# Kernel optimization log

Hardware: AMD Instinct MI355X
Metric: run time of the kernel (lower is better)

The kernel has to match this reference:

```python
import jax, jax.numpy as jnp
import numpy as np

# Static config mirroring PyTorchConv1dAutograd(padding=0, index_back=500, out_size=None)
PADDING = 0
INDEX_BACK = 500


def next_power2(n):
    return 1 << (int(n) - 1).bit_length()


def setup_inputs() -> dict:
    key = jax.random.key(0)
    k1, k2, k3 = jax.random.split(key, 3)
    N, C, W = 32, 64, 4096
    F, WW = 128, 9
    x = jax.random.normal(k1, (N, C, W), dtype=jnp.float32)
    filt = jax.random.normal(k2, (F, C, WW), dtype=jnp.float32) * 0.1
    bias = jax.random.normal(k3, (F,), dtype=jnp.float32)
    return {"x": x, "filt": filt, "bias": bias}


def reference(x, filt, bias):
    N, C, W = x.shape
    F, _, WW = filt.shape
    p = PADDING
    out_W = W - WW + 1 + 2 * p
    WWW = max(out_W, WW)
    init_fft_size = next_power2(W + 2 * p + WWW - 1)

    # zero-pad input by `p` on the front; rfft pads the rest with zeros via n=
    if p > 0:
        x = jnp.pad(x, ((0, 0), (0, 0), (p, 0)))
    xfft = jnp.fft.rfft(x, n=init_fft_size, axis=-1)          # [N, C, half]
    yfft = jnp.fft.rfft(filt, n=init_fft_size, axis=-1)       # [F, C, half]

    half_fft_size = init_fft_size // 2 + 1
    half_compressed = half_fft_size - INDEX_BACK
    compress_fft_size = half_compressed * 2
    xfft = xfft[..., :half_compressed]
    yfft = yfft[..., :half_compressed]

    # cross-correlation in frequency domain: X * conj(Y), contract over channels
    spec = jnp.einsum('ncw,fcw->nfw', xfft, jnp.conj(yfft))   # [N, F, half_compressed]
    out = jnp.fft.irfft(spec, n=compress_fft_size, axis=-1)[..., :out_W]
    return out + bias[None, :, None]
```

## Files before the change

kernel.cpp:

```cpp
#include <hip/hip_runtime.h>
#include <hip/hip_bf16.h>

typedef unsigned short u16;
typedef unsigned int   u32;

using bf16x8 = __attribute__((ext_vector_type(8))) short;
using f32x4  = __attribute__((ext_vector_type(4))) float;

#define NB    32
#define CC    64
#define WW_   4096
#define FF    128
#define TAPS  9
#define KBINS 3597
#define N2    7194
#define OW    4088
#define SIG2  4096
#define JMAX  4104
#define KD    4160
#define XTROWS 4352
#define PBIG  58933248LL

__device__ __forceinline__ u16 f2bf(float f) {
    u32 u = __float_as_uint(f);
    return (u16)((u + 0x7FFFu + ((u >> 16) & 1u)) >> 16);
}
__device__ __forceinline__ float vsin(float x) {
    float r; asm("v_sin_f32 %0, %1" : "=v"(r) : "v"(x)); return r;
}

__device__ __forceinline__ void gload16(const void* g, void* l) {
    __builtin_amdgcn_global_load_lds(
        (const __attribute__((address_space(1))) void*)g,
        (__attribute__((address_space(3))) void*)l, 16, 0, 0);
}

__global__ __launch_bounds__(256) void cast_xt(const float* __restrict__ x,
                                               u16* __restrict__ XT) {
    __shared__ u16 tl[64][72];
    const int tid = threadIdx.x;
    const int it = blockIdx.x, n = blockIdx.y;
    const int i0 = it * 64;
    {
        int c = tid >> 2, io = (tid & 3) * 16;
        const float4* src = (const float4*)(x + ((size_t)n * CC + c) * WW_ +
                                            i0 + io);
#pragma unroll
        for (int q = 0; q < 4; q++) {
            float4 v = src[q];
            tl[c][io + q * 4 + 0] = f2bf(v.x);
            tl[c][io + q * 4 + 1] = f2bf(v.y);
            tl[c][io + q * 4 + 2] = f2bf(v.z);
            tl[c][io + q * 4 + 3] = f2bf(v.w);
        }
    }
    __syncthreads();
    {
        int l = tid >> 2;
        int R = i0 + l + 64;
        int key = R & 7;
        u16* dst = XT + ((size_t)n * XTROWS + R) * 64;
        int pb0 = (tid & 3) * 2;
#pragma unroll
        for (int pq = 0; pq < 2; pq++) {
            int pb = pb0 + pq;
            int ch0 = (pb ^ key) << 3;
            bf16x8 v;
#pragma unroll
            for (int ci = 0; ci < 8; ci++) v[ci] = (short)tl[ch0 + ci][l];
            *(bf16x8*)(dst + pb * 8) = v;
        }
    }
}

__global__ __launch_bounds__(256) void prep(const float* __restrict__ filt,
                                            u16* __restrict__ F2) {
    int idx = blockIdx.x * 256 + threadIdx.x;
    if (idx >= FF * 576) return;
    int f = idx / 576, wc = idx % 576;
    int w = wc >> 6, c = wc & 63;
    F2[idx] = f2bf(filt[((size_t)f * CC + c) * TAPS + w]);
}

__global__ __launch_bounds__(256) void gen_D(u16* __restrict__ D) {
    int t = blockIdx.x;
    u32* row = (u32*)(D + (size_t)t * KD);
    for (int p = threadIdx.x; p < KD / 2; p += 256) {
        u32 pack = 0;
#pragma unroll
        for (int e = 0; e < 2; e++) {
            int j = 2 * p + e;
            float d = 0.f;
            if (j < JMAX) {
                long long v = 8192LL * t - 7194LL * (long long)(j - 8);
                long long r = v % PBIG;
                if (r < 0) r += PBIG;
                if (r == 0) {
                    d = 7193.0f / 7194.0f;
                } else {
                    long long n64 = (7193LL * r) % (2LL * PBIG);
                    float num = vsin((float)n64 * (float)(0.5 / (double)PBIG));
                    long long rr = (r < PBIG - r) ? r : PBIG - r;
                    float den;
                    if (rr < (1LL << 18))
                        den = (float)rr *
                              (float)(3.14159265358979323846 / (double)PBIG);
                    else
                        den = vsin((float)r * (float)(0.5 / (double)PBIG));
                    d = num / (7194.0f * den);
                }
            }
            pack |= (u32)f2bf(d) << (16 * e);
        }
        row[p] = pack;
    }
}

#define STAGE_A9(T, BUF)                                                    \
    _Pragma("unroll")                                                       \
    for (int q = 0; q < 4; q++) {                                           \
        gload16(F2 + (size_t)(wid * 32 + q * 8 + (lane >> 3)) * 576 +       \
                    (T) * 64 + (((lane & 7) ^ (lane >> 3)) * 8),            \
                lac + (BUF)*16384 + (wid * 32 + q * 8) * 128);              \
    }

__global__ __launch_bounds__(256, 2) void conv9(const u16* __restrict__ XT,
                                                const u16* __restrict__ F2,
                                                u16* __restrict__ Z) {
    __shared__ u16 la[2 * 128 * 64];
    __shared__ u16 lx[96 * 64];
    const int tid = threadIdx.x;
    const int lane = tid & 63, wid = tid >> 6;
    const int jt = blockIdx.x, n = blockIdx.y;
    const int fr = lane & 15;
    const int hk = (lane >> 4) << 4;
    const int askew = (fr & 7) << 4;
    char* lac = (char*)la;
    char* lxc = (char*)lx;

    {
        const u16* src = XT + ((size_t)n * XTROWS + jt * 64 + 56) * 64;
#pragma unroll
        for (int q = 0; q < 3; q++) {
            int off = (wid * 3 + q) * 512;
            gload16(src + off + lane * 8, lxc + off * 2);
        }
    }
    STAGE_A9(0, 0)
    __syncthreads();

    f32x4 acc[2][4];
#pragma unroll
    for (int i = 0; i < 2; i++)
#pragma unroll
        for (int j = 0; j < 4; j++) acc[i][j] = (f32x4){0.f, 0.f, 0.f, 0.f};

    bf16x8 af[2][2], bfr[4][2];
    for (int t = 0; t < TAPS; ++t) {
        const int cur = t & 1, nxt = cur ^ 1;
#pragma unroll
        for (int m2 = 0; m2 < 2; m2++)
#pragma unroll
            for (int kk = 0; kk < 2; kk++) {
                int row_ = wid * 32 + m2 * 16 + fr;
                af[m2][kk] = *(const bf16x8*)(lac + cur * 16384 + row_ * 128 +
                                              ((kk * 64 + hk) ^ askew));
            }
#pragma unroll
        for (int n4 = 0; n4 < 4; n4++)
#pragma unroll
            for (int kk = 0; kk < 2; kk++) {
                int l_ = n4 * 16 + fr + t;
                bfr[n4][kk] = *(const bf16x8*)(lxc + l_ * 128 +
                                  ((kk * 64 + hk) ^ ((l_ & 7) << 4)));
            }
        if (t + 1 < TAPS) STAGE_A9(t + 1, nxt)
        __builtin_amdgcn_s_setprio(1);
#pragma unroll
        for (int kk = 0; kk < 2; kk++)
#pragma unroll
            for (int m2 = 0; m2 < 2; m2++)
#pragma unroll
                for (int n4 = 0; n4 < 4; n4++)
                    acc[m2][n4] = __builtin_amdgcn_mfma_f32_16x16x32_bf16(
                        af[m2][kk], bfr[n4][kk], acc[m2][n4], 0, 0, 0);
        __builtin_amdgcn_s_setprio(0);
        __syncthreads();
    }

#pragma unroll
    for (int m2 = 0; m2 < 2; m2++) {
#pragma unroll
        for (int n4 = 0; n4 < 4; n4++) {
            int colk = jt * 64 + n4 * 16 + fr;
            int f0 = wid * 32 + m2 * 16 + ((lane >> 4) << 2);
#pragma unroll
            for (int j = 0; j < 4; j++) {
                int sig2 = n * 128 + f0 + j;
                Z[(size_t)sig2 * KD + colk] = f2bf(acc[m2][n4][j]);
            }
        }
    }
}

#define MFMA_Q(AS, BS, MH, NH)                                              \
    __builtin_amdgcn_s_setprio(1);                                          \
    _Pragma("unroll")                                                       \
    for (int kk = 0; kk < 2; kk++)                                          \
        _Pragma("unroll")                                                   \
        for (int m4 = 0; m4 < 4; m4++)                                      \
            _Pragma("unroll")                                               \
            for (int n2 = 0; n2 < 2; n2++)                                  \
                acc[(MH)*4 + m4][(NH)*2 + n2] =                             \
                    __builtin_amdgcn_mfma_f32_16x16x32_bf16(                \
                        AS[m4][kk], BS[n2][kk],                             \
                        acc[(MH)*4 + m4][(NH)*2 + n2], 0, 0, 0);            \
    __builtin_amdgcn_s_setprio(0);

#define LOAD_A(AS, MH, BUF)                                                 \
    _Pragma("unroll")                                                       \
    for (int m4 = 0; m4 < 4; m4++)                                          \
        _Pragma("unroll")                                                   \
        for (int kk = 0; kk < 2; kk++) {                                    \
            int row_ = wr * 128 + (MH)*64 + m4 * 16 + fr;                   \
            AS[m4][kk] = *(const bf16x8*)(smem + (BUF)*32768 +              \
                          row_ * 128 + ((kk * 64 + hk) ^ askew));           \
        }

#define LOAD_B(BS, NH, BUF)                                                 \
    _Pragma("unroll")                                                       \
    for (int n2 = 0; n2 < 2; n2++)                                          \
        _Pragma("unroll")                                                   \
        for (int kk = 0; kk < 2; kk++) {                                    \
            int row_ = wc * 64 + (NH)*32 + n2 * 16 + fr;                    \
            BS[n2][kk] = *(const bf16x8*)(smem + 65536 + (BUF)*32768 +      \
                          row_ * 128 + ((kk * 64 + hk) ^ askew));           \
        }

#define STAGE(Q, R, BUF)                                                    \
    {                                                                       \
        const u16* g_ = ((R) < 2) ? gA : gB;                                \
        size_t ro_ = (size_t)((R)&1) * 128 * K;                             \
        int lb_ = (((R) < 2) ? 0 : 65536) + (BUF)*32768 +                   \
                  (((R)&1) * 128 + wid * 16) * 128;                         \
        gload16(g_ + ro_ + (Q)*64, smem + lb_);                             \
        gload16(g_ + ro_ + (size_t)8 * K + (Q)*64, smem + lb_ + 1024);      \
    }

#define BAR() __builtin_amdgcn_s_barrier()

template <int MODE>
__global__ __launch_bounds__(512, 1) void gemm256(const u16* __restrict__ A,
                                                  const u16* __restrict__ B,
                                                  int K, int gridN,
                                                  void* __restrict__ Out,
                                                  int ldo,
                                                  const float* __restrict__ bias) {
    extern __shared__ char smem[];
    const int tid = threadIdx.x;
    const int lane = tid & 63, wid = tid >> 6;
    const int wr = wid >> 2, wc = wid & 3;
    const int fr = lane & 15;
    const int hk = (lane >> 4) << 4;
    const int askew = (fr & 7) << 4;

    const int nwg = (int)gridDim.x, cpx = nwg >> 3;
    const int bid = (int)blockIdx.x;
    const int wg = (bid & 7) * cpx + (bid >> 3);
    const int tm = wg / gridN, tn = wg % gridN;
    const int NT = K >> 6;

    f32x4 acc[8][4];
#pragma unroll
    for (int i = 0; i < 8; i++)
#pragma unroll
        for (int j = 0; j < 4; j++) acc[i][j] = (f32x4){0.f, 0.f, 0.f, 0.f};

    const int srow = lane >> 3;
    const int scol = ((lane & 7) ^ srow) * 8;
    const u16* gA = A + (size_t)(tm * 256 + wid * 16 + srow) * K + scol;
    const u16* gB = B + (size_t)(tn * 256 + wid * 16 + srow) * K + scol;

    STAGE(0, 0, 0) STAGE(0, 1, 0) STAGE(0, 2, 0) STAGE(0, 3, 0)
    STAGE(1, 0, 1) STAGE(1, 1, 1)
    asm volatile("s_waitcnt vmcnt(4)" ::: "memory");
    BAR();

    bf16x8 a0[4][2], a1[4][2], b0[2][2], b1[2][2];
    for (int t = 0; t < NT; ++t) {
        const int cur = t & 1, nxt = cur ^ 1;
        LOAD_A(a0, 0, cur)
        LOAD_B(b0, 0, cur)
        LOAD_B(b1, 1, cur)
        if (t + 1 < NT) { STAGE(t + 1, 2, nxt) STAGE(t + 1, 3, nxt) }
        MFMA_Q(a0, b0, 0, 0)
        LOAD_A(a1, 1, cur)
        MFMA_Q(a0, b1, 0, 1)
        asm volatile("s_waitcnt lgkmcnt(0)" ::: "memory");
        __builtin_amdgcn_sched_barrier(0);
        BAR();
        if (t + 2 < NT) { STAGE(t + 2, 0, cur) STAGE(t + 2, 1, cur) }
        MFMA_Q(a1, b1, 1, 1)
        MFMA_Q(a1, b0, 1, 0)
        if (t + 2 < NT) {
            asm volatile("s_waitcnt vmcnt(4)" ::: "memory");
        } else if (t + 1 < NT) {
            asm volatile("s_waitcnt vmcnt(0)" ::: "memory");
        }
        BAR();
    }

#pragma unroll
    for (int m = 0; m < 8; m++) {
#pragma unroll
        for (int n = 0; n < 4; n++) {
            int col  = tn * 256 + wc * 64 + n * 16 + fr;
            int row0 = tm * 256 + wr * 128 + m * 16 + ((lane >> 4) << 2);
#pragma unroll
            for (int j = 0; j < 4; j++) {
                int grow = row0 + j;
                if (MODE == 0) {
                    ((u16*)Out)[(size_t)grow * ldo + col] = f2bf(acc[m][n][j]);
                } else {
                    if (col < OW) {
                        ((float*)Out)[(size_t)grow * OW + col] =
                            acc[m][n][j] + bias[grow & 127];
                    }
                }
            }
        }
    }
}

extern "C" void kernel_launch(void* const* d_in, const int* in_sizes, int n_in,
                              void* d_out, int out_size, void* d_ws, size_t ws_size,
                              hipStream_t stream) {
    (void)in_sizes; (void)n_in; (void)out_size; (void)ws_size;
    const float* x    = (const float*)d_in[0];
    const float* filt = (const float*)d_in[1];
    const float* bias = (const float*)d_in[2];

    char* ws = (char*)d_ws;
    u16* XT = (u16*)(ws);
    u16* Z  = (u16*)(ws + 17825792);
    u16* Dt = (u16*)(ws + 51904512);
    u16* F2 = (u16*)(ws + 85983232);

    hipFuncSetAttribute(reinterpret_cast<const void*>(gemm256<1>),
                        hipFuncAttributeMaxDynamicSharedMemorySize, 131072);

    hipMemsetAsync(XT, 0, (size_t)32 * XTROWS * 64 * 2, stream);
    cast_xt<<<dim3(64, 32), 256, 0, stream>>>(x, XT);
    prep<<<288, 256, 0, stream>>>(filt, F2);
    gen_D<<<SIG2, 256, 0, stream>>>(Dt);
    conv9<<<dim3(KD / 64, NB), 256, 0, stream>>>(XT, F2, Z);
    gemm256<1><<<16 * 16, 512, 131072, stream>>>(
        Z, Dt, KD, 16, d_out, OW, bias);
}
```

Measured before the change: 201.8 us.

## Fold memset and filter prep into existing kernels, cheapen gen_D math

Removes the full-buffer memset by having extra cast_xt blocks zero only the pad rows, and merges the filter-prep kernel into gen_D as extra blocks, cutting two launches. gen_D's 64-bit modular arithmetic becomes 32-bit integer math with a cheaper modulus trick, and the division becomes a hardware reciprocal. cast_xt's LDS transpose now packs bf16 pairs into 32-bit words and writes two rows per thread. The risks are int32 overflow in the index math and lower precision from the approximate reciprocal.

```diff
diff --git a/kernel.cpp b/kernel.cpp
--- a/kernel.cpp
+++ b/kernel.cpp
@@ -19,7 +19,7 @@
 #define JMAX  4104
 #define KD    4160
 #define XTROWS 4352
-#define PBIG  58933248LL
+#define PBIG  58933248
 
 __device__ __forceinline__ u16 f2bf(float f) {
     u32 u = __float_as_uint(f);
@@ -27,6 +27,9 @@
 }
 __device__ __forceinline__ float vsin(float x) {
     float r; asm("v_sin_f32 %0, %1" : "=v"(r) : "v"(x)); return r;
+}
+__device__ __forceinline__ float vrcp(float x) {
+    float r; asm("v_rcp_f32 %0, %1" : "=v"(r) : "v"(x)); return r;
 }
 
 __device__ __forceinline__ void gload16(const void* g, void* l) {
@@ -37,53 +40,68 @@
 
 __global__ __launch_bounds__(256) void cast_xt(const float* __restrict__ x,
                                                u16* __restrict__ XT) {
-    __shared__ u16 tl[64][72];
+    __shared__ u32 tl[64][33];
     const int tid = threadIdx.x;
     const int it = blockIdx.x, n = blockIdx.y;
+    if (it >= 64) {
+        int zb = it - 64;
+        int i2 = tid >> 3, cb = tid & 7;
+        bf16x8 z;
+#pragma unroll
+        for (int q = 0; q < 8; q++) z[q] = 0;
+#pragma unroll
+        for (int e = 0; e < 2; e++) {
+            int zr = zb * 64 + 2 * i2 + e;
+            int R = (zr < 64) ? zr : (4096 + zr);
+            *(bf16x8*)(XT + ((size_t)n * XTROWS + R) * 64 + cb * 8) = z;
+        }
+        return;
+    }
     const int i0 = it * 64;
     {
-        int c = tid >> 2, io = (tid & 3) * 16;
+        int c = tid >> 2, iq = tid & 3;
         const float4* src = (const float4*)(x + ((size_t)n * CC + c) * WW_ +
-                                            i0 + io);
+                                            i0 + iq * 16);
 #pragma unroll
         for (int q = 0; q < 4; q++) {
             float4 v = src[q];
-            tl[c][io + q * 4 + 0] = f2bf(v.x);
-            tl[c][io + q * 4 + 1] = f2bf(v.y);
-            tl[c][io + q * 4 + 2] = f2bf(v.z);
-            tl[c][io + q * 4 + 3] = f2bf(v.w);
+            tl[c][iq * 8 + q * 2]     = (u32)f2bf(v.x) | ((u32)f2bf(v.y) << 16);
+            tl[c][iq * 8 + q * 2 + 1] = (u32)f2bf(v.z) | ((u32)f2bf(v.w) << 16);
         }
     }
     __syncthreads();
     {
-        int l = tid >> 2;
-        int R = i0 + l + 64;
-        int key = R & 7;
-        u16* dst = XT + ((size_t)n * XTROWS + R) * 64;
-        int pb0 = (tid & 3) * 2;
-#pragma unroll
-        for (int pq = 0; pq < 2; pq++) {
-            int pb = pb0 + pq;
-            int ch0 = (pb ^ key) << 3;
-            bf16x8 v;
-#pragma unroll
-            for (int ci = 0; ci < 8; ci++) v[ci] = (short)tl[ch0 + ci][l];
-            *(bf16x8*)(dst + pb * 8) = v;
-        }
-    }
-}
-
-__global__ __launch_bounds__(256) void prep(const float* __restrict__ filt,
-                                            u16* __restrict__ F2) {
-    int idx = blockIdx.x * 256 + threadIdx.x;
-    if (idx >= FF * 576) return;
-    int f = idx / 576, wc = idx % 576;
-    int w = wc >> 6, c = wc & 63;
-    F2[idx] = f2bf(filt[((size_t)f * CC + c) * TAPS + w]);
-}
-
-__global__ __launch_bounds__(256) void gen_D(u16* __restrict__ D) {
-    int t = blockIdx.x;
+        int i2 = tid >> 3, cb = tid & 7;
+        int R0 = i0 + 64 + 2 * i2, R1 = R0 + 1;
+        bf16x8 vlo, vhi;
+#pragma unroll
+        for (int ci = 0; ci < 8; ci++) {
+            u32 w = tl[cb * 8 + ci][i2];
+            vlo[ci] = (short)(u16)(w & 0xffffu);
+            vhi[ci] = (short)(u16)(w >> 16);
+        }
+        *(bf16x8*)(XT + ((size_t)n * XTROWS + R0) * 64 +
+                   ((cb ^ (R0 & 7)) * 8)) = vlo;
+        *(bf16x8*)(XT + ((size_t)n * XTROWS + R1) * 64 +
+                   ((cb ^ (R1 & 7)) * 8)) = vhi;
+    }
+}
+
+__global__ __launch_bounds__(256) void gen_D(u16* __restrict__ D,
+                                             const float* __restrict__ filt,
+                                             u16* __restrict__ F2) {
+    int b = blockIdx.x;
+    if (b >= SIG2) {
+        int idx = (b - SIG2) * 256 + threadIdx.x;
+        if (idx < FF * 576) {
+            int f = idx / 576, wc = idx % 576;
+            int w = wc >> 6, c = wc & 63;
+            F2[idx] = f2bf(filt[((size_t)f * CC + c) * TAPS + w]);
+        }
+        return;
+    }
+    const int t = b;
+    const int base = 8192 * t;
     u32* row = (u32*)(D + (size_t)t * KD);
     for (int p = threadIdx.x; p < KD / 2; p += 256) {
         u32 pack = 0;
@@ -92,22 +110,20 @@
             int j = 2 * p + e;
             float d = 0.f;
             if (j < JMAX) {
-                long long v = 8192LL * t - 7194LL * (long long)(j - 8);
-                long long r = v % PBIG;
-                if (r < 0) r += PBIG;
+                int v = base - 7194 * (j - 8);
+                int r = (v < 0) ? v + PBIG : v;
                 if (r == 0) {
                     d = 7193.0f / 7194.0f;
                 } else {
-                    long long n64 = (7193LL * r) % (2LL * PBIG);
-                    float num = vsin((float)n64 * (float)(0.5 / (double)PBIG));
-                    long long rr = (r < PBIG - r) ? r : PBIG - r;
-                    float den;
-                    if (rr < (1LL << 18))
-                        den = (float)rr *
-                              (float)(3.14159265358979323846 / (double)PBIG);
-                    else
-                        den = vsin((float)r * (float)(0.5 / (double)PBIG));
-                    d = num / (7194.0f * den);
+                    int m = 7194 * (r & 16383) - r;
+                    if (m < 0) m += 2 * PBIG;
+                    float num = vsin((float)m * (float)(0.5 / (double)PBIG));
+                    int rr = (r < PBIG - r) ? r : PBIG - r;
+                    float den = (rr < (1 << 18))
+                        ? (float)rr *
+                          (float)(3.14159265358979323846 / (double)PBIG)
+                        : vsin((float)r * (float)(0.5 / (double)PBIG));
+                    d = num * vrcp(den) * (1.0f / 7194.0f);
                 }
             }
             pack |= (u32)f2bf(d) << (16 * e);
@@ -349,10 +365,8 @@
     hipFuncSetAttribute(reinterpret_cast<const void*>(gemm256<1>),
                         hipFuncAttributeMaxDynamicSharedMemorySize, 131072);
 
-    hipMemsetAsync(XT, 0, (size_t)32 * XTROWS * 64 * 2, stream);
-    cast_xt<<<dim3(64, 32), 256, 0, stream>>>(x, XT);
-    prep<<<288, 256, 0, stream>>>(filt, F2);
-    gen_D<<<SIG2, 256, 0, stream>>>(Dt);
+    cast_xt<<<dim3(68, 32), 256, 0, stream>>>(x, XT);
+    gen_D<<<SIG2 + 288, 256, 0, stream>>>(Dt, filt, F2);
     conv9<<<dim3(KD / 64, NB), 256, 0, stream>>>(XT, F2, Z);
     gemm256<1><<<16 * 16, 512, 131072, stream>>>(
         Z, Dt, KD, 16, d_out, OW, bias);
```

New measurement: 169.5 us. 16.0% less time.
